# Kernel optimization log

Measured on AMD Instinct MI355X. Metric: run time of the kernel, lower is better.

The kernel has to match this reference:

```python
import jax, jax.numpy as jnp
import numpy as np

N = 50000       # num nodes
E = 800000      # num edges
F_NODE = 128    # input node feature dim
F_EDGE = 32     # input edge feature dim
H = 64          # hidden dim (heads=1)
NEG_SLOPE = 0.2 # GAT leaky-relu slope


def _segment_softmax(scores, seg, num_segments):
    # numerically stable softmax over edges grouped by destination node
    m = jax.ops.segment_max(scores, seg, num_segments=num_segments)
    ex = jnp.exp(scores - m[seg])
    denom = jax.ops.segment_sum(ex, seg, num_segments=num_segments)
    return ex / (denom[seg] + 1e-16)


def _egat_conv(x, src, dst, eattr, W, We, a_src, a_dst, a_e, b):
    # PyG-style GAT layer with edge features (heads=1, no self loops).
    xp = x @ W                      # [N, H] projected nodes
    ep = eattr @ We                 # [E, H] projected edges (returned as new edge feats)
    score = (xp @ a_src)[src] + (xp @ a_dst)[dst] + ep @ a_e  # [E]
    score = jax.nn.leaky_relu(score, NEG_SLOPE)
    alpha = _segment_softmax(score, dst, N)                    # [E]
    out = jax.ops.segment_sum(alpha[:, None] * xp[src], dst, num_segments=N) + b
    return out, alpha, ep


def setup_inputs() -> dict:
    key = jax.random.key(0)
    ks = jax.random.split(key, 24)
    inp = {
        "x": jax.random.normal(ks[0], (N, F_NODE), jnp.float32),
        "edge_index": jax.random.randint(ks[1], (2, E), 0, N, jnp.int64),
        "edge_attr": jax.random.normal(ks[2], (E, F_EDGE), jnp.float32),
    }
    def glorot(k, shape):
        fan = shape[0] + shape[-1]
        return jax.random.normal(k, shape, jnp.float32) * jnp.sqrt(2.0 / fan)
    dims = [(F_NODE, F_EDGE), (H, H), (H, H)]
    i = 3
    for li, (din, dedge) in enumerate(dims, start=1):
        inp[f"W{li}"] = glorot(ks[i], (din, H)); i += 1
        inp[f"We{li}"] = glorot(ks[i], (dedge, H)); i += 1
        inp[f"as{li}"] = glorot(ks[i], (H,)); i += 1
        inp[f"ad{li}"] = glorot(ks[i], (H,)); i += 1
        inp[f"ae{li}"] = glorot(ks[i], (H,)); i += 1
        inp[f"b{li}"] = jnp.zeros((H,), jnp.float32)
    inp["Wc"] = glorot(ks[i], (H, 1)); i += 1
    inp["bc"] = jnp.zeros((1,), jnp.float32)
    return inp


def reference(x, edge_index, edge_attr,
              W1, We1, as1, ad1, ae1, b1,
              W2, We2, as2, ad2, ae2, b2,
              W3, We3, as3, ad3, ae3, b3,
              Wc, bc):
    src, dst = edge_index[0], edge_index[1]
    # layer 1 (edge feats projected F_EDGE -> H, reused as next edge_attr)
    x1, _, e1 = _egat_conv(x, src, dst, edge_attr, W1, We1, as1, ad1, ae1, b1)
    x1 = jax.nn.relu(x1)  # dropout is identity in eval mode
    # layer 2
    x2, _, e2 = _egat_conv(x1, src, dst, e1, W2, We2, as2, ad2, ae2, b2)
    x2 = jax.nn.relu(x2)
    # layer 3
    x3, _, _ = _egat_conv(x2, src, dst, e2, W3, We3, as3, ad3, ae3, b3)
    x3 = jax.nn.relu(x3)
    return x3 @ Wc + bc  # [N, 1]
```

## Files before the change

kernel.cpp:

```cpp
#include <hip/hip_runtime.h>
#include <hip/hip_fp16.h>
#include <math.h>

#define NN 50000
#define NE 800000
#define FN 128
#define FE 32
#define HD 64
#define NBKT 196
#define EPB 2048
#define NSB ((NE + EPB - 1) / EPB)
#define EPT (EPB / 256)
#define CNT_N (NBKT * NSB)
#define SCB 2048
#define NB2 ((CNT_N + SCB - 1) / SCB)
#define GP ((NN + 127) / 128)

typedef unsigned long long u64;
typedef unsigned short u16;

__device__ __forceinline__ u64 make_trec(const float* __restrict__ eattr,
                                         const float* __restrict__ v123,
                                         int s, int e) {
  const float4* ea = (const float4*)(eattr + (size_t)e * FE);
  float a = 0.f, b = 0.f, c = 0.f;
#pragma unroll
  for (int q = 0; q < FE / 4; ++q) {
    float4 xv = ea[q];
    const float* v1 = v123 + q * 4;
    const float* v2 = v123 + 32 + q * 4;
    const float* v3 = v123 + 64 + q * 4;
    a += xv.x * v1[0] + xv.y * v1[1] + xv.z * v1[2] + xv.w * v1[3];
    b += xv.x * v2[0] + xv.y * v2[1] + xv.z * v2[2] + xv.w * v2[3];
    c += xv.x * v3[0] + xv.y * v3[1] + xv.z * v3[2] + xv.w * v3[3];
  }
  return (u64)(u16)s
       | ((u64)__half_as_ushort(__float2half_rn(a)) << 16)
       | ((u64)__half_as_ushort(__float2half_rn(b)) << 32)
       | ((u64)__half_as_ushort(__float2half_rn(c)) << 48);
}

__global__ __launch_bounds__(256) void k_count(
    const int* __restrict__ dstA, int* __restrict__ cnt,
    const float* __restrict__ We1, const float* __restrict__ We2,
    const float* __restrict__ We3, const float* __restrict__ ae1,
    const float* __restrict__ ae2, const float* __restrict__ ae3,
    float* __restrict__ v123) {
  __shared__ int hist[NBKT];
  const int t = threadIdx.x;
  const int blk = blockIdx.x;
  if (t < NBKT) hist[t] = 0;
  __syncthreads();
  const int base = blk * EPB;
#pragma unroll 1
  for (int it = 0; it < EPT; ++it) {
    int e = base + it * 256 + t;
    if (e < NE) atomicAdd(&hist[dstA[e] >> 8], 1);
  }
  __syncthreads();
  if (t < NBKT) cnt[t * NSB + blk] = hist[t];

  if (blk != 0) return;
  __shared__ float u2[HD], u3[HD], u23[HD];
  if (t < HD) {
    float s2 = 0.f, s3 = 0.f;
    for (int j = 0; j < HD; ++j) {
      s2 += We2[t * HD + j] * ae2[j];
      s3 += We3[t * HD + j] * ae3[j];
    }
    u2[t] = s2; u3[t] = s3;
  }
  __syncthreads();
  if (t < HD) {
    float s23 = 0.f;
    for (int j = 0; j < HD; ++j) s23 += We2[t * HD + j] * u3[j];
    u23[t] = s23;
  }
  __syncthreads();
  if (t < FE) {
    float a = 0.f, b = 0.f, c = 0.f;
    for (int j = 0; j < HD; ++j) {
      float w = We1[t * HD + j];
      a += w * ae1[j];
      b += w * u2[j];
      c += w * u23[j];
    }
    v123[t] = a; v123[32 + t] = b; v123[64 + t] = c;
  }
}

__global__ __launch_bounds__(256) void k_scanA2(const int* __restrict__ cnt,
                                                int* __restrict__ bsum) {
  __shared__ int ws[4];
  const int t = threadIdx.x, lane = t & 63, wid = t >> 6;
  const int i0 = blockIdx.x * SCB + t * 8;
  int s = 0;
#pragma unroll
  for (int j = 0; j < 8; ++j) {
    int i = i0 + j;
    if (i < CNT_N) s += cnt[i];
  }
#pragma unroll
  for (int off = 32; off; off >>= 1) s += __shfl_xor(s, off);
  if (lane == 0) ws[wid] = s;
  __syncthreads();
  if (t == 0) bsum[blockIdx.x] = ws[0] + ws[1] + ws[2] + ws[3];
}

__global__ __launch_bounds__(256) void k_scanB2(int* __restrict__ cnt,
                                                const int* __restrict__ bsum) {
  __shared__ int blockOff;
  __shared__ int wOff[4];
  const int b = blockIdx.x;
  const int t = threadIdx.x, lane = t & 63, wid = t >> 6;
  if (t < 64) {
    int v = (t < NB2) ? bsum[t] : 0;
    int p = v;
#pragma unroll
    for (int off = 1; off < 64; off <<= 1) {
      int u = __shfl_up(p, off);
      if (lane >= off) p += u;
    }
    if (t == b) blockOff = p - v;
  }
  __syncthreads();
  const int i0 = b * SCB + t * 8;
  int v[8];
#pragma unroll
  for (int j = 0; j < 8; ++j) {
    int i = i0 + j;
    v[j] = (i < CNT_N) ? cnt[i] : 0;
  }
  int s = 0;
#pragma unroll
  for (int j = 0; j < 8; ++j) s += v[j];
  int p = s;
#pragma unroll
  for (int off = 1; off < 64; off <<= 1) {
    int u = __shfl_up(p, off);
    if (lane >= off) p += u;
  }
  if (lane == 63) wOff[wid] = p;
  __syncthreads();
  int woff = 0;
  for (int wq = 0; wq < wid; ++wq) woff += wOff[wq];
  int excl = blockOff + woff + (p - s);
#pragma unroll
  for (int j = 0; j < 8; ++j) {
    int i = i0 + j;
    if (i < CNT_N) { cnt[i] = excl; excl += v[j]; }
  }
}

__global__ __launch_bounds__(256) void k_mega3(
    const float* __restrict__ x, const float* __restrict__ W,
    const float* __restrict__ asv, const float* __restrict__ adv,
    __half* __restrict__ xph, float* __restrict__ ssrc, float* __restrict__ sdst,
    const int* __restrict__ srcA, const int* __restrict__ dstA,
    const float* __restrict__ eattr, const float* __restrict__ v123,
    const int* __restrict__ gbase, u64* __restrict__ btrec,
    u16* __restrict__ bdst) {
  __shared__ int off[NBKT];
  const int t = threadIdx.x;
  if (blockIdx.x < NSB) {
    const int blk = blockIdx.x;
    if (t < NBKT) off[t] = gbase[t * NSB + blk];
    __syncthreads();
    const int base = blk * EPB;
#pragma unroll 1
    for (int it = 0; it < EPT; ++it) {
      int e = base + it * 256 + t;
      if (e < NE) {
        int d = dstA[e];
        int s = srcA[e];
        u64 r = make_trec(eattr, v123, s, e);
        int pos = atomicAdd(&off[d >> 8], 1);
        btrec[pos] = r;
        bdst[pos] = (u16)(d & 255);
      }
    }
    return;
  }
  const int pb = blockIdx.x - NSB;
  const int w = t >> 6, l = t & 63;
  const int g = w * 4 + (l >> 4);
  const int rr = g * 8;
  const int c0 = (l & 15) * 4;
  const int row0 = pb * 128;

  int xoff[8];
#pragma unroll
  for (int i = 0; i < 8; ++i) {
    int gr = row0 + rr + i;
    xoff[i] = (gr < NN ? gr : NN - 1) * FN;
  }

  float acc[8][4];
#pragma unroll
  for (int i = 0; i < 8; ++i)
#pragma unroll
    for (int j = 0; j < 4; ++j) acc[i][j] = 0.f;

  for (int k = 0; k < FN; k += 4) {
    float wv[4][4];
#pragma unroll
    for (int kk = 0; kk < 4; ++kk) {
      float4 wq = *(const float4*)(W + (k + kk) * HD + c0);
      wv[kk][0] = wq.x; wv[kk][1] = wq.y; wv[kk][2] = wq.z; wv[kk][3] = wq.w;
    }
#pragma unroll
    for (int i = 0; i < 8; ++i) {
      float4 a = *(const float4*)(x + xoff[i] + k);
#pragma unroll
      for (int j = 0; j < 4; ++j)
        acc[i][j] += a.x * wv[0][j] + a.y * wv[1][j] + a.z * wv[2][j] + a.w * wv[3][j];
    }
  }

  float as4[4], ad4[4];
#pragma unroll
  for (int j = 0; j < 4; ++j) { as4[j] = asv[c0 + j]; ad4[j] = adv[c0 + j]; }
#pragma unroll
  for (int i = 0; i < 8; ++i) {
    int gr = row0 + rr + i;
    float ps = 0.f, pd = 0.f;
#pragma unroll
    for (int j = 0; j < 4; ++j) {
      ps += acc[i][j] * as4[j];
      pd += acc[i][j] * ad4[j];
    }
#pragma unroll
    for (int off2 = 1; off2 < 16; off2 <<= 1) {
      ps += __shfl_xor(ps, off2);
      pd += __shfl_xor(pd, off2);
    }
    if (gr < NN) {
      union { __half2 h2[2]; float2 f2; } u;
      u.h2[0] = __floats2half2_rn(acc[i][0], acc[i][1]);
      u.h2[1] = __floats2half2_rn(acc[i][2], acc[i][3]);
      *(float2*)(xph + (size_t)gr * HD + c0) = u.f2;
      if ((l & 15) == 0) { ssrc[gr] = ps; sdst[gr] = pd; }
    }
  }
}

__global__ __launch_bounds__(256) void k_bucket(
    const int* __restrict__ gbase, const u64* __restrict__ btrec,
    const u16* __restrict__ bdst, int* __restrict__ row_ptr,
    u64* __restrict__ aos) {
  __shared__ int hist[256], off2[256];
  __shared__ int wsum[4];
  const int b = blockIdx.x;
  const int t = threadIdx.x, lane = t & 63, wid = t >> 6;
  const int s = gbase[b * NSB];
  const int e = (b + 1 < NBKT) ? gbase[(b + 1) * NSB] : NE;
  hist[t] = 0;
  __syncthreads();
  for (int p = s + t; p < e; p += 256) atomicAdd(&hist[(int)bdst[p]], 1);
  __syncthreads();
  int v = hist[t];
  int pfx = v;
#pragma unroll
  for (int o = 1; o < 64; o <<= 1) {
    int u = __shfl_up(pfx, o);
    if (lane >= o) pfx += u;
  }
  if (lane == 63) wsum[wid] = pfx;
  __syncthreads();
  int woff = 0;
  for (int wq = 0; wq < wid; ++wq) woff += wsum[wq];
  const int excl = woff + pfx - v;
  off2[t] = excl;
  const int n = b * 256 + t;
  if (n < NN) row_ptr[n] = s + excl;
  if (b == 0 && t == 0) row_ptr[NN] = NE;
  __syncthreads();
  for (int p = s + t; p < e; p += 256) {
    u64 r = btrec[p];
    int d8 = (int)bdst[p];
    int pos = s + atomicAdd(&off2[d8], 1);
    aos[pos] = r;
  }
}

template <int TSEL>
__global__ __launch_bounds__(256) void k_agg_proj(
    const int* __restrict__ row_ptr, const u64* __restrict__ aos,
    const __half* __restrict__ xin, const float* __restrict__ ssrc_in,
    const float* __restrict__ sdst_in, const float* __restrict__ bias,
    const float* __restrict__ Wn, const float* __restrict__ asn,
    const float* __restrict__ adn, __half* __restrict__ xout,
    float* __restrict__ ssrc_out, float* __restrict__ sdst_out) {
  __shared__ __half swh[HD * HD];
  const int t = threadIdx.x;
  for (int i = t; i < HD * HD; i += 256) swh[i] = __float2half_rn(Wn[i]);

  const int gw = (blockIdx.x * blockDim.x + t) >> 6;
  const int lane = t & 63;
  const int g = lane >> 3;
  const int q = lane & 7;
  const int n = gw * 8 + g;
  const bool act = n < NN;
  int beg = 0, end = 0;
  float sd = 0.f;
  if (act) { beg = row_ptr[n]; end = row_ptr[n + 1]; sd = sdst_in[n]; }

  float dsum = 0.f;
  float4 o0 = make_float4(0.f, 0.f, 0.f, 0.f);
  float4 o1 = make_float4(0.f, 0.f, 0.f, 0.f);
  for (int base = beg; base < end; base += 16) {
    const int p0 = base + q, p1 = base + 8 + q;
    float pe0 = 0.f, pe1 = 0.f;
    int s0 = 0, s1 = 0;
    if (p0 < end) {
      u64 r = aos[p0];
      s0 = (int)(r & 0xFFFFu);
      float tt = __half2float(__ushort_as_half((u16)((r >> (16 * TSEL)) & 0xFFFFu)));
      float raw = ssrc_in[s0] + sd + tt;
      raw = raw > 0.f ? raw : 0.2f * raw;
      pe0 = __expf(raw);
    }
    if (p1 < end) {
      u64 r = aos[p1];
      s1 = (int)(r & 0xFFFFu);
      float tt = __half2float(__ushort_as_half((u16)((r >> (16 * TSEL)) & 0xFFFFu)));
      float raw = ssrc_in[s1] + sd + tt;
      raw = raw > 0.f ? raw : 0.2f * raw;
      pe1 = __expf(raw);
    }
    dsum += pe0 + pe1;
#pragma unroll
    for (int j = 0; j < 8; ++j) {
      const int sl = g * 8 + j;
      float pa = __shfl(pe0, sl);
      int sa = __shfl(s0, sl);
      float pb = __shfl(pe1, sl);
      int sb = __shfl(s1, sl);
      union { float4 f4; __half2 h2[4]; } ua, ub;
      ua.f4 = ((const float4*)(xin + (size_t)sa * HD))[q];
      ub.f4 = ((const float4*)(xin + (size_t)sb * HD))[q];
      float2 a0 = __half22float2(ua.h2[0]);
      float2 a1 = __half22float2(ua.h2[1]);
      float2 a2 = __half22float2(ua.h2[2]);
      float2 a3 = __half22float2(ua.h2[3]);
      o0.x += pa * a0.x; o0.y += pa * a0.y; o0.z += pa * a1.x; o0.w += pa * a1.y;
      o1.x += pa * a2.x; o1.y += pa * a2.y; o1.z += pa * a3.x; o1.w += pa * a3.y;
      float2 b0 = __half22float2(ub.h2[0]);
      float2 b1 = __half22float2(ub.h2[1]);
      float2 b2 = __half22float2(ub.h2[2]);
      float2 b3 = __half22float2(ub.h2[3]);
      o0.x += pb * b0.x; o0.y += pb * b0.y; o0.z += pb * b1.x; o0.w += pb * b1.y;
      o1.x += pb * b2.x; o1.y += pb * b2.y; o1.z += pb * b3.x; o1.w += pb * b3.y;
    }
  }
#pragma unroll
  for (int off = 1; off < 8; off <<= 1) dsum += __shfl_xor(dsum, off);

  const float inv = 1.f / (dsum + 1e-16f);
  const float4 b0 = ((const float4*)bias)[q * 2];
  const float4 b1 = ((const float4*)bias)[q * 2 + 1];
  float vreg[8];
  vreg[0] = fmaxf(o0.x * inv + b0.x, 0.f);
  vreg[1] = fmaxf(o0.y * inv + b0.y, 0.f);
  vreg[2] = fmaxf(o0.z * inv + b0.z, 0.f);
  vreg[3] = fmaxf(o0.w * inv + b0.w, 0.f);
  vreg[4] = fmaxf(o1.x * inv + b1.x, 0.f);
  vreg[5] = fmaxf(o1.y * inv + b1.y, 0.f);
  vreg[6] = fmaxf(o1.z * inv + b1.z, 0.f);
  vreg[7] = fmaxf(o1.w * inv + b1.w, 0.f);

  __syncthreads();

  float out8[8] = {0.f, 0.f, 0.f, 0.f, 0.f, 0.f, 0.f, 0.f};
#pragma unroll
  for (int kq = 0; kq < 8; ++kq) {
#pragma unroll
    for (int m = 0; m < 8; ++m) {
      float vb = __shfl(vreg[m], (lane & 56) | kq);
      union { float4 f4; __half2 h2[4]; } uw;
      uw.f4 = *(const float4*)(swh + (kq * 8 + m) * HD + q * 8);
      float2 w0 = __half22float2(uw.h2[0]);
      float2 w1 = __half22float2(uw.h2[1]);
      float2 w2 = __half22float2(uw.h2[2]);
      float2 w3 = __half22float2(uw.h2[3]);
      out8[0] += vb * w0.x; out8[1] += vb * w0.y;
      out8[2] += vb * w1.x; out8[3] += vb * w1.y;
      out8[4] += vb * w2.x; out8[5] += vb * w2.y;
      out8[6] += vb * w3.x; out8[7] += vb * w3.y;
    }
  }

  float ps = 0.f, pd = 0.f;
#pragma unroll
  for (int j = 0; j < 8; ++j) {
    ps += out8[j] * asn[q * 8 + j];
    pd += out8[j] * adn[q * 8 + j];
  }
#pragma unroll
  for (int off = 1; off < 8; off <<= 1) {
    ps += __shfl_xor(ps, off);
    pd += __shfl_xor(pd, off);
  }

  if (!act) return;
  union { float4 f4; __half2 h2[4]; } wv;
  wv.h2[0] = __floats2half2_rn(out8[0], out8[1]);
  wv.h2[1] = __floats2half2_rn(out8[2], out8[3]);
  wv.h2[2] = __floats2half2_rn(out8[4], out8[5]);
  wv.h2[3] = __floats2half2_rn(out8[6], out8[7]);
  ((float4*)(xout + (size_t)n * HD))[q] = wv.f4;
  if (q == 0) { ssrc_out[n] = ps; sdst_out[n] = pd; }
}

template <int TSEL>
__global__ __launch_bounds__(256) void k_agg_head(
    const int* __restrict__ row_ptr, const u64* __restrict__ aos,
    const __half* __restrict__ xin, const float* __restrict__ ssrc_in,
    const float* __restrict__ sdst_in, const float* __restrict__ bias,
    const float* __restrict__ Wc, const float* __restrict__ bc,
    float* __restrict__ outf) {
  const int gw = (blockIdx.x * blockDim.x + threadIdx.x) >> 6;
  const int lane = threadIdx.x & 63;
  const int g = lane >> 3;
  const int q = lane & 7;
  const int n = gw * 8 + g;
  const bool act = n < NN;
  int beg = 0, end = 0;
  float sd = 0.f;
  if (act) { beg = row_ptr[n]; end = row_ptr[n + 1]; sd = sdst_in[n]; }

  float dsum = 0.f;
  float4 o0 = make_float4(0.f, 0.f, 0.f, 0.f);
  float4 o1 = make_float4(0.f, 0.f, 0.f, 0.f);
  for (int base = beg; base < end; base += 16) {
    const int p0 = base + q, p1 = base + 8 + q;
    float pe0 = 0.f, pe1 = 0.f;
    int s0 = 0, s1 = 0;
    if (p0 < end) {
      u64 r = aos[p0];
      s0 = (int)(r & 0xFFFFu);
      float tt = __half2float(__ushort_as_half((u16)((r >> (16 * TSEL)) & 0xFFFFu)));
      float raw = ssrc_in[s0] + sd + tt;
      raw = raw > 0.f ? raw : 0.2f * raw;
      pe0 = __expf(raw);
    }
    if (p1 < end) {
      u64 r = aos[p1];
      s1 = (int)(r & 0xFFFFu);
      float tt = __half2float(__ushort_as_half((u16)((r >> (16 * TSEL)) & 0xFFFFu)));
      float raw = ssrc_in[s1] + sd + tt;
      raw = raw > 0.f ? raw : 0.2f * raw;
      pe1 = __expf(raw);
    }
    dsum += pe0 + pe1;
#pragma unroll
    for (int j = 0; j < 8; ++j) {
      const int sl = g * 8 + j;
      float pa = __shfl(pe0, sl);
      int sa = __shfl(s0, sl);
      float pb = __shfl(pe1, sl);
      int sb = __shfl(s1, sl);
      union { float4 f4; __half2 h2[4]; } ua, ub;
      ua.f4 = ((const float4*)(xin + (size_t)sa * HD))[q];
      ub.f4 = ((const float4*)(xin + (size_t)sb * HD))[q];
      float2 a0 = __half22float2(ua.h2[0]);
      float2 a1 = __half22float2(ua.h2[1]);
      float2 a2 = __half22float2(ua.h2[2]);
      float2 a3 = __half22float2(ua.h2[3]);
      o0.x += pa * a0.x; o0.y += pa * a0.y; o0.z += pa * a1.x; o0.w += pa * a1.y;
      o1.x += pa * a2.x; o1.y += pa * a2.y; o1.z += pa * a3.x; o1.w += pa * a3.y;
      float2 b0 = __half22float2(ub.h2[0]);
      float2 b1 = __half22float2(ub.h2[1]);
      float2 b2 = __half22float2(ub.h2[2]);
      float2 b3 = __half22float2(ub.h2[3]);
      o0.x += pb * b0.x; o0.y += pb * b0.y; o0.z += pb * b1.x; o0.w += pb * b1.y;
      o1.x += pb * b2.x; o1.y += pb * b2.y; o1.z += pb * b3.x; o1.w += pb * b3.y;
    }
  }
#pragma unroll
  for (int off = 1; off < 8; off <<= 1) dsum += __shfl_xor(dsum, off);

  if (!act) return;
  const float inv = 1.f / (dsum + 1e-16f);
  const float4 b0 = ((const float4*)bias)[q * 2];
  const float4 b1 = ((const float4*)bias)[q * 2 + 1];
  const float4 w0 = ((const float4*)Wc)[q * 2];
  const float4 w1 = ((const float4*)Wc)[q * 2 + 1];
  float c = fmaxf(o0.x * inv + b0.x, 0.f) * w0.x +
            fmaxf(o0.y * inv + b0.y, 0.f) * w0.y +
            fmaxf(o0.z * inv + b0.z, 0.f) * w0.z +
            fmaxf(o0.w * inv + b0.w, 0.f) * w0.w +
            fmaxf(o1.x * inv + b1.x, 0.f) * w1.x +
            fmaxf(o1.y * inv + b1.y, 0.f) * w1.y +
            fmaxf(o1.z * inv + b1.z, 0.f) * w1.z +
            fmaxf(o1.w * inv + b1.w, 0.f) * w1.w;
#pragma unroll
  for (int off = 1; off < 8; off <<= 1) c += __shfl_xor(c, off);
  if (q == 0) outf[n] = c + bc[0];
}

extern "C" void kernel_launch(void* const* d_in, const int* in_sizes, int n_in,
                              void* d_out, int out_size, void* d_ws, size_t ws_size,
                              hipStream_t stream) {
  const float* x     = (const float*)d_in[0];
  const int*   ei    = (const int*)d_in[1];
  const float* eattr = (const float*)d_in[2];
  const float* W1  = (const float*)d_in[3];
  const float* We1 = (const float*)d_in[4];
  const float* as1 = (const float*)d_in[5];
  const float* ad1 = (const float*)d_in[6];
  const float* ae1 = (const float*)d_in[7];
  const float* b1  = (const float*)d_in[8];
  const float* W2  = (const float*)d_in[9];
  const float* We2 = (const float*)d_in[10];
  const float* as2 = (const float*)d_in[11];
  const float* ad2 = (const float*)d_in[12];
  const float* ae2 = (const float*)d_in[13];
  const float* b2  = (const float*)d_in[14];
  const float* W3  = (const float*)d_in[15];
  const float* We3 = (const float*)d_in[16];
  const float* as3 = (const float*)d_in[17];
  const float* ad3 = (const float*)d_in[18];
  const float* ae3 = (const float*)d_in[19];
  const float* b3  = (const float*)d_in[20];
  const float* Wc  = (const float*)d_in[21];
  const float* bc  = (const float*)d_in[22];

  const int* srcA = ei;
  const int* dstA = ei + NE;
  float* outf = (float*)d_out;

  char* w = (char*)d_ws;
  auto alloc = [&](size_t bytes) {
    char* p = w;
    w += (bytes + 255) & ~(size_t)255;
    return p;
  };
  float* v123 = (float*)alloc(96 * 4);
  u64* aos = (u64*)alloc((size_t)NE * 8);
  u64* btrec = (u64*)alloc((size_t)NE * 8);
  u16* bdst = (u16*)alloc((size_t)NE * 2);
  int* row_ptr = (int*)alloc((size_t)(NN + 1) * 4);
  int* cnt = (int*)alloc((size_t)CNT_N * 4);
  int* bsum = (int*)alloc((size_t)NB2 * 4);
  __half* xpA = (__half*)alloc((size_t)NN * HD * 2);
  __half* xpB = (__half*)alloc((size_t)NN * HD * 2);
  float* ssrcA = (float*)alloc((size_t)NN * 4);
  float* sdstA = (float*)alloc((size_t)NN * 4);
  float* ssrcB = (float*)alloc((size_t)NN * 4);
  float* sdstB = (float*)alloc((size_t)NN * 4);

  const int gA = ((NN + 7) / 8 * 64 + 255) / 256;

  k_count<<<NSB, 256, 0, stream>>>(dstA, cnt, We1, We2, We3, ae1, ae2, ae3, v123);
  k_scanA2<<<NB2, 256, 0, stream>>>(cnt, bsum);
  k_scanB2<<<NB2, 256, 0, stream>>>(cnt, bsum);
  k_mega3<<<NSB + GP, 256, 0, stream>>>(x, W1, as1, ad1, xpA, ssrcA, sdstA,
                                        srcA, dstA, eattr, v123, cnt, btrec, bdst);
  k_bucket<<<NBKT, 256, 0, stream>>>(cnt, btrec, bdst, row_ptr, aos);
  k_agg_proj<1><<<gA, 256, 0, stream>>>(row_ptr, aos, xpA, ssrcA, sdstA, b1,
                                        W2, as2, ad2, xpB, ssrcB, sdstB);
  k_agg_proj<2><<<gA, 256, 0, stream>>>(row_ptr, aos, xpB, ssrcB, sdstB, b2,
                                        W3, as3, ad3, xpA, ssrcA, sdstA);
  k_agg_head<3><<<gA, 256, 0, stream>>>(row_ptr, aos, xpA, ssrcA, sdstA, b3,
                                        Wc, bc, outf);
}
```

Baseline: 171.3 us.

## Stage bucket scatter through shared memory and coalesce edge-attribute dot products

The scatter half of the fused kernel now has 8 lanes cooperate on each edge's 32-float attribute row, loading float4 slices and reducing the three dot products with xor-shuffles, so eattr reads are coalesced. Records are first sorted by bucket in shared memory using a local histogram and scan, then written to global memory in bucket-contiguous runs instead of as scattered per-edge atomic writes. This adds shared-memory usage (about 22KB), extra barriers and shuffle work, which may lower occupancy for the projection blocks that share this kernel.

Result: faster. 153.1 us (-10.6%).

```diff
diff --git a/kernel.cpp b/kernel.cpp
--- a/kernel.cpp
+++ b/kernel.cpp
@@ -18,27 +18,7 @@
 
 typedef unsigned long long u64;
 typedef unsigned short u16;
-
-__device__ __forceinline__ u64 make_trec(const float* __restrict__ eattr,
-                                         const float* __restrict__ v123,
-                                         int s, int e) {
-  const float4* ea = (const float4*)(eattr + (size_t)e * FE);
-  float a = 0.f, b = 0.f, c = 0.f;
-#pragma unroll
-  for (int q = 0; q < FE / 4; ++q) {
-    float4 xv = ea[q];
-    const float* v1 = v123 + q * 4;
-    const float* v2 = v123 + 32 + q * 4;
-    const float* v3 = v123 + 64 + q * 4;
-    a += xv.x * v1[0] + xv.y * v1[1] + xv.z * v1[2] + xv.w * v1[3];
-    b += xv.x * v2[0] + xv.y * v2[1] + xv.z * v2[2] + xv.w * v2[3];
-    c += xv.x * v3[0] + xv.y * v3[1] + xv.z * v3[2] + xv.w * v3[3];
-  }
-  return (u64)(u16)s
-       | ((u64)__half_as_ushort(__float2half_rn(a)) << 16)
-       | ((u64)__half_as_ushort(__float2half_rn(b)) << 32)
-       | ((u64)__half_as_ushort(__float2half_rn(c)) << 48);
-}
+typedef unsigned char u8;
 
 __global__ __launch_bounds__(256) void k_count(
     const int* __restrict__ dstA, int* __restrict__ cnt,
@@ -152,7 +132,7 @@
   }
 }
 
-__global__ __launch_bounds__(256) void k_mega3(
+__global__ __launch_bounds__(256) void k_mega5(
     const float* __restrict__ x, const float* __restrict__ W,
     const float* __restrict__ asv, const float* __restrict__ adv,
     __half* __restrict__ xph, float* __restrict__ ssrc, float* __restrict__ sdst,
@@ -160,24 +140,96 @@
     const float* __restrict__ eattr, const float* __restrict__ v123,
     const int* __restrict__ gbase, u64* __restrict__ btrec,
     u16* __restrict__ bdst) {
-  __shared__ int off[NBKT];
+  __shared__ u64 strec[EPB];
+  __shared__ u16 sdst16[EPB];
+  __shared__ u8 sbkt[EPB];
+  __shared__ int h[256];
+  __shared__ int cur[256];
+  __shared__ int lb0[256];
+  __shared__ int gb[NBKT];
+  __shared__ int wsum[4];
   const int t = threadIdx.x;
   if (blockIdx.x < NSB) {
     const int blk = blockIdx.x;
-    if (t < NBKT) off[t] = gbase[t * NSB + blk];
+    const int base = blk * EPB;
+    h[t] = 0;
+    if (t < NBKT) gb[t] = gbase[t * NSB + blk];
     __syncthreads();
-    const int base = blk * EPB;
-#pragma unroll 1
-    for (int it = 0; it < EPT; ++it) {
-      int e = base + it * 256 + t;
-      if (e < NE) {
-        int d = dstA[e];
-        int s = srcA[e];
-        u64 r = make_trec(eattr, v123, s, e);
-        int pos = atomicAdd(&off[d >> 8], 1);
-        btrec[pos] = r;
-        bdst[pos] = (u16)(d & 255);
+    const int w = t >> 6, lane = t & 63;
+    const int g = lane >> 3, q = lane & 7;
+    const float4 v1q = *(const float4*)(v123 + q * 4);
+    const float4 v2q = *(const float4*)(v123 + 32 + q * 4);
+    const float4 v3q = *(const float4*)(v123 + 64 + q * 4);
+    const int perm = 8 * q + g;
+    u64 tr[8];
+    int dl[8];
+#pragma unroll
+    for (int it = 0; it < 8; ++it) {
+      const int E0 = base + (w * 8 + it) * 64;
+      tr[it] = 0; dl[it] = -1;
+      if (E0 < NE) {
+        const int e = E0 + perm;
+        const int d = dstA[e];
+        const int s = srcA[e];
+        float ra = 0.f, rb = 0.f, rc = 0.f;
+#pragma unroll
+        for (int k = 0; k < 8; ++k) {
+          const float4 xv =
+              *(const float4*)(eattr + (size_t)(E0 + 8 * k + g) * FE + q * 4);
+          float a = xv.x * v1q.x + xv.y * v1q.y + xv.z * v1q.z + xv.w * v1q.w;
+          float b = xv.x * v2q.x + xv.y * v2q.y + xv.z * v2q.z + xv.w * v2q.w;
+          float c = xv.x * v3q.x + xv.y * v3q.y + xv.z * v3q.z + xv.w * v3q.w;
+#pragma unroll
+          for (int off = 1; off < 8; off <<= 1) {
+            a += __shfl_xor(a, off);
+            b += __shfl_xor(b, off);
+            c += __shfl_xor(c, off);
+          }
+          if (q == k) { ra = a; rb = b; rc = c; }
+        }
+        tr[it] = (u64)(u16)s
+               | ((u64)__half_as_ushort(__float2half_rn(ra)) << 16)
+               | ((u64)__half_as_ushort(__float2half_rn(rb)) << 32)
+               | ((u64)__half_as_ushort(__float2half_rn(rc)) << 48);
+        dl[it] = d;
+        atomicAdd(&h[d >> 8], 1);
       }
+    }
+    __syncthreads();
+    {
+      int v = h[t];
+      int p = v;
+#pragma unroll
+      for (int o = 1; o < 64; o <<= 1) {
+        int u = __shfl_up(p, o);
+        if (lane >= o) p += u;
+      }
+      if (lane == 63) wsum[w] = p;
+      __syncthreads();
+      int woff = 0;
+      for (int wq = 0; wq < w; ++wq) woff += wsum[wq];
+      const int excl = woff + p - v;
+      cur[t] = excl;
+      lb0[t] = excl;
+    }
+    __syncthreads();
+#pragma unroll
+    for (int it = 0; it < 8; ++it) {
+      if (dl[it] >= 0) {
+        const int b = dl[it] >> 8;
+        const int pos = atomicAdd(&cur[b], 1);
+        strec[pos] = tr[it];
+        sdst16[pos] = (u16)(dl[it] & 255);
+        sbkt[pos] = (u8)b;
+      }
+    }
+    __syncthreads();
+    const int nval = min(EPB, NE - base);
+    for (int p = t; p < nval; p += 256) {
+      const int b = (int)sbkt[p];
+      const int gpos = gb[b] + (p - lb0[b]);
+      btrec[gpos] = strec[p];
+      bdst[gpos] = sdst16[p];
     }
     return;
   }
@@ -555,7 +607,7 @@
   k_count<<<NSB, 256, 0, stream>>>(dstA, cnt, We1, We2, We3, ae1, ae2, ae3, v123);
   k_scanA2<<<NB2, 256, 0, stream>>>(cnt, bsum);
   k_scanB2<<<NB2, 256, 0, stream>>>(cnt, bsum);
-  k_mega3<<<NSB + GP, 256, 0, stream>>>(x, W1, as1, ad1, xpA, ssrcA, sdstA,
+  k_mega5<<<NSB + GP, 256, 0, stream>>>(x, W1, as1, ad1, xpA, ssrcA, sdstA,
                                         srcA, dstA, eattr, v123, cnt, btrec, bdst);
   k_bucket<<<NBKT, 256, 0, stream>>>(cnt, btrec, bdst, row_ptr, aos);
   k_agg_proj<1><<<gA, 256, 0, stream>>>(row_ptr, aos, xpA, ssrcA, sdstA, b1,
```
